# Optimization experiments

Hardware: AMD Instinct MI355X
Metric: run time of the kernel (lower is better)

The kernel has to match this reference:

```python
import jax, jax.numpy as jnp
import numpy as np
from jax.scipy.special import gammaln

# dims: S=state_dim, A=act_dim, H=horizon, HY=hyper_dim, B=batch, T=seq len
S, A, H, HY, B, T = 256, 16, 30, 64, 64, 64
EPS = 1e-6


def setup_inputs() -> dict:
    key = jax.random.key(0)
    ks = jax.random.split(key, 9)
    logp_o = jax.nn.log_softmax(jax.random.normal(ks[0], (T, B, S)), axis=-1)
    logp_u = jax.nn.log_softmax(jax.random.normal(ks[1], (T, B, A)), axis=-1)
    value = jax.random.normal(ks[2], (H, B, A, S))
    z = jax.random.normal(ks[3], (B, HY))
    b = jax.nn.softmax(jax.random.normal(ks[4], (B, S)), axis=-1)
    # learned parameters (xavier-ish scales, matching torch init magnitudes)
    w = jax.random.normal(ks[5], (1, A, S, S)) * (2.0 / (S + S)) ** 0.5
    w_offset_w = jax.random.normal(ks[6], (A * S * S, HY)) * 0.01  # Linear weight * 0.1
    tau = jax.random.uniform(ks[7], (1, 1), minval=-1.0, maxval=1.0)
    tau_offset_w = jax.random.normal(ks[8], (1, HY)) * 0.01
    return {"logp_o": logp_o, "logp_u": logp_u, "value": value, "z": z, "b": b,
            "w": w, "w_offset_w": w_offset_w, "tau": tau, "tau_offset_w": tau_offset_w}


def rectify(x):
    # positive rate; clipped exp for numerical safety
    return jnp.exp(jnp.clip(x, -8.0, 8.0))


def poisson_pdf(rate, K):
    # truncated, renormalized Poisson pmf over horizons 1..K; rate: [B,1] -> [B,K]
    ks = jnp.arange(1, K + 1, dtype=rate.dtype)
    logp = ks * jnp.log(rate) - rate - gammaln(ks + 1.0)
    return jax.nn.softmax(logp, axis=-1)


def reference(logp_o, logp_u, value, z, b, w, w_offset_w, tau, tau_offset_w):
    # compute_transition: hyper-offset + base full-rank weights, softmax over next-state
    w_off = (z @ w_offset_w.T).reshape(B, A, S, S)
    transition = jax.nn.softmax(w_off + w, axis=-1)  # [B,A,S,S]

    # compute_horizon_dist
    rate = rectify(tau + z @ tau_offset_w.T)  # [B,1]
    h_dist = poisson_pdf(rate, H)             # [B,H]

    # update_action for all timesteps at once
    alpha_a = jax.nn.softmax(logp_u, axis=-1)  # [T,B,A]

    def plan(b_t):
        # [B,S] x [H,B,A,S] -> [H,B,A]
        logits = jnp.einsum('bi,hbki->hbk', b_t, value)
        a = jax.nn.softmax(logits, axis=-1)
        return jnp.einsum('hbk,bh->bk', a, h_dist)  # [B,A]

    def step(b_t, inp):
        lo_t, a_t = inp
        # update_belief
        s_next = jnp.einsum('bkij,bi,bk->bj', transition, b_t, a_t)  # [B,S]
        b_next = jax.nn.softmax(jnp.log(s_next + EPS) + lo_t, axis=-1)
        return b_next, (b_next, plan(b_next))

    _, (alpha_b, alpha_pi) = jax.lax.scan(step, b, (logp_o, alpha_a))
    return alpha_b, alpha_pi  # [T,B,S], [T,B,A]
```

## Files before the change

### kernel.cpp

```cpp
#include <hip/hip_runtime.h>
#include <hip/hip_fp16.h>

#define DS 256
#define DA 16
#define DH 30
#define DHY 64
#define DB 64
#define DT 64

union HV  { int4 i4; __half2 h2[4]; };
union HV2 { int2 i2; __half2 h2[2]; };
typedef _Float16 f16x8 __attribute__((ext_vector_type(8)));
typedef float f32x4 __attribute__((ext_vector_type(4)));


__global__ __launch_bounds__(64) void k_hdist(const float* __restrict__ z,
                                              const float* __restrict__ tau,
                                              const float* __restrict__ tauw,
                                              float* __restrict__ h_dist) {
  const int bb = threadIdx.x;
  if (bb >= DB) return;
  float x = tau[0];
  for (int hy = 0; hy < DHY; ++hy) x = fmaf(z[bb * DHY + hy], tauw[hy], x);
  x = fminf(fmaxf(x, -8.f), 8.f);
  const float rate = __expf(x);
  const float lr = x;
  float lp[DH];
  float lg = 0.f;
  float mx = -1e30f;
  #pragma unroll
  for (int h = 0; h < DH; ++h) {
    const float ks = (float)(h + 1);
    lg += __logf(ks);
    lp[h] = ks * lr - rate - lg;
    mx = fmaxf(mx, lp[h]);
  }
  float sum = 0.f;
  #pragma unroll
  for (int h = 0; h < DH; ++h) { lp[h] = __expf(lp[h] - mx); sum += lp[h]; }
  const float inv = 1.f / sum;
  #pragma unroll
  for (int h = 0; h < DH; ++h) h_dist[bb * DH + h] = lp[h] * inv;
}

__global__ __launch_bounds__(256) void k_zf16(const float* __restrict__ z,
                                              _Float16* __restrict__ zf) {
  const int i = blockIdx.x * 256 + threadIdx.x;
  if (i < DB * DHY) zf[i] = (_Float16)z[i];
}

__global__ __launch_bounds__(256) void k_alpha(const float* __restrict__ logp_u,
                                               float* __restrict__ alpha_a) {
  const int row = blockIdx.x * 16 + (threadIdx.x >> 4);
  const int k = threadIdx.x & 15;
  const float v = logp_u[(size_t)row * DA + k];
  float m = v;
  #pragma unroll
  for (int o = 8; o >= 1; o >>= 1) m = fmaxf(m, __shfl_xor(m, o, 16));
  const float e = __expf(v - m);
  float s = e;
  #pragma unroll
  for (int o = 8; o >= 1; o >>= 1) s += __shfl_xor(s, o, 16);
  alpha_a[(size_t)row * DA + k] = e / s;
}

__global__ __launch_bounds__(256) void k_zero(float* __restrict__ out_pi) {
  out_pi[blockIdx.x * 256 + threadIdx.x] = 0.f;
}

__global__ __launch_bounds__(256) void k_vconv(const float* __restrict__ v,
                                               __half* __restrict__ v16, int n4) {
  const int stride = gridDim.x * 256;
  for (int i = blockIdx.x * 256 + threadIdx.x; i < n4; i += stride) {
    const float4 f = reinterpret_cast<const float4*>(v)[i];
    reinterpret_cast<__half2*>(v16)[2 * i]     = __floats2half2_rn(f.x, f.y);
    reinterpret_cast<__half2*>(v16)[2 * i + 1] = __floats2half2_rn(f.z, f.w);
  }
}

__global__ __launch_bounds__(256) void k_trans(const float* __restrict__ w,
                                               const float* __restrict__ wofs,
                                               const _Float16* __restrict__ zf,
                                               __half* __restrict__ trans) {
  const int ki = blockIdx.x;
  const int t = threadIdx.x;
  const int l = t & 63;
  const int wv = t >> 6;
  __shared__ __align__(16) char smem[32 * 1024];

  {
    const float* wrow = wofs + (size_t)ki * (DS * DHY);
    const int q = t & 3;
    #pragma unroll
    for (int pass = 0; pass < 4; ++pass) {
      const int j = pass * 64 + (t >> 2);
      const float4* src = reinterpret_cast<const float4*>(wrow + (size_t)j * DHY + q * 16);
      const float4 f0 = src[0], f1 = src[1], f2 = src[2], f3 = src[3];
      __half2 h[8];
      h[0] = __floats2half2_rn(f0.x, f0.y); h[1] = __floats2half2_rn(f0.z, f0.w);
      h[2] = __floats2half2_rn(f1.x, f1.y); h[3] = __floats2half2_rn(f1.z, f1.w);
      h[4] = __floats2half2_rn(f2.x, f2.y); h[5] = __floats2half2_rn(f2.z, f2.w);
      h[6] = __floats2half2_rn(f3.x, f3.y); h[7] = __floats2half2_rn(f3.z, f3.w);
      const int4* hv = reinterpret_cast<const int4*>(h);
      int b0 = j * 128 + (q * 2) * 16;     b0 ^= ((j & 7) << 4);
      int b1 = j * 128 + (q * 2 + 1) * 16; b1 ^= ((j & 7) << 4);
      *reinterpret_cast<int4*>(smem + b0) = hv[0];
      *reinterpret_cast<int4*>(smem + b1) = hv[1];
    }
  }
  __syncthreads();

  const int bcol = wv * 16 + (l & 15);
  const f16x8 Bf0 = *reinterpret_cast<const f16x8*>(zf + bcol * DHY + 0  + (l >> 4) * 8);
  const f16x8 Bf1 = *reinterpret_cast<const f16x8*>(zf + bcol * DHY + 32 + (l >> 4) * 8);

  f32x4 acc[16];
  #pragma unroll
  for (int m = 0; m < 16; ++m) {
    const int row0 = m * 16 + (l >> 4) * 4;
    const float4 w4 = *reinterpret_cast<const float4*>(w + (size_t)ki * DS + row0);
    acc[m][0] = w4.x; acc[m][1] = w4.y; acc[m][2] = w4.z; acc[m][3] = w4.w;
  }
  #pragma unroll
  for (int m = 0; m < 16; ++m) {
    const int row = m * 16 + (l & 15);
    int ba = row * 128 + (l >> 4) * 16;        ba ^= ((row & 7) << 4);
    int bb = row * 128 + (4 + (l >> 4)) * 16;  bb ^= ((row & 7) << 4);
    const f16x8 a0 = *reinterpret_cast<const f16x8*>(smem + ba);
    const f16x8 a1 = *reinterpret_cast<const f16x8*>(smem + bb);
    acc[m] = __builtin_amdgcn_mfma_f32_16x16x32_f16(a0, Bf0, acc[m], 0, 0, 0);
    acc[m] = __builtin_amdgcn_mfma_f32_16x16x32_f16(a1, Bf1, acc[m], 0, 0, 0);
  }

  float ssum = 0.f;
  #pragma unroll
  for (int m = 0; m < 16; ++m) {
    acc[m][0] = __expf(acc[m][0]); acc[m][1] = __expf(acc[m][1]);
    acc[m][2] = __expf(acc[m][2]); acc[m][3] = __expf(acc[m][3]);
    ssum += (acc[m][0] + acc[m][1]) + (acc[m][2] + acc[m][3]);
  }
  ssum += __shfl_xor(ssum, 16, 64);
  ssum += __shfl_xor(ssum, 32, 64);
  const float inv = 1.f / ssum;

  __half* tb = trans + (size_t)bcol * (DA * DS * DS) + (size_t)ki * DS;
  #pragma unroll
  for (int m = 0; m < 16; ++m) {
    const int j0 = m * 16 + (l >> 4) * 4;
    union { int2 i2; __half2 h[2]; } o;
    o.h[0] = __floats2half2_rn(acc[m][0] * inv, acc[m][1] * inv);
    o.h[1] = __floats2half2_rn(acc[m][2] * inv, acc[m][3] * inv);
    *reinterpret_cast<int2*>(tb + j0) = o.i2;
  }
}

__global__ __launch_bounds__(256) void k_mbuild(const __half* __restrict__ trans,
                                                const float* __restrict__ alpha_a,
                                                __half* __restrict__ Mch,
                                                int t0, int TC) {
  const int b = blockIdx.x >> 4;
  const int ich = (blockIdx.x & 15) << 4;
  const int tid = threadIdx.x;
  const int lane = tid & 63;
  const int wid = tid >> 6;
  __shared__ __half2 a_lds[16 * DA];
  for (int r = tid; r < TC * DA; r += 256)
    a_lds[r] = __float2half2_rn(alpha_a[((size_t)(t0 + (r >> 4)) * DB + b) * DA + (r & 15)]);
  __syncthreads();
  for (int io = 0; io < 4; ++io) {
    const int i = ich + io * 4 + wid;
    const __half* tp = trans + ((size_t)b * DA * DS + i) * DS + lane * 4;
    __half2 T2[32];
    #pragma unroll
    for (int k = 0; k < 16; ++k) {
      HV2 u;
      u.i2 = *reinterpret_cast<const int2*>(tp + (size_t)k * (DS * DS));
      T2[2 * k]     = u.h2[0];
      T2[2 * k + 1] = u.h2[1];
    }
    const __half2 z2 = __float2half2_rn(0.f);
    for (int tt = 0; tt < TC; ++tt) {
      __half2 m0 = z2, m1 = z2;
      #pragma unroll
      for (int k = 0; k < 16; ++k) {
        const __half2 ak = a_lds[tt * DA + k];
        m0 = __hfma2(ak, T2[2 * k], m0);
        m1 = __hfma2(ak, T2[2 * k + 1], m1);
      }
      HV2 o;
      o.h2[0] = m0;
      o.h2[1] = m1;
      *reinterpret_cast<int2*>(Mch + (((size_t)tt * DB + b) * DS + i) * DS + lane * 4) = o.i2;
    }
  }
}

#define LBAR() asm volatile("s_waitcnt lgkmcnt(0)\n\ts_barrier" ::: "memory")

#define SC_ISSUE(S, T)                                                          \
  if ((T) < TC) {                                                               \
    const __half* mb_ = Mch + (((size_t)(T) * DB + b) << 16) + jg * 8;          \
    S##0 = *reinterpret_cast<const int4*>(mb_ + (size_t)(iq + 0 * 32) * DS);    \
    S##1 = *reinterpret_cast<const int4*>(mb_ + (size_t)(iq + 1 * 32) * DS);    \
    S##2 = *reinterpret_cast<const int4*>(mb_ + (size_t)(iq + 2 * 32) * DS);    \
    S##3 = *reinterpret_cast<const int4*>(mb_ + (size_t)(iq + 3 * 32) * DS);    \
    S##4 = *reinterpret_cast<const int4*>(mb_ + (size_t)(iq + 4 * 32) * DS);    \
    S##5 = *reinterpret_cast<const int4*>(mb_ + (size_t)(iq + 5 * 32) * DS);    \
    S##6 = *reinterpret_cast<const int4*>(mb_ + (size_t)(iq + 6 * 32) * DS);    \
    S##7 = *reinterpret_cast<const int4*>(mb_ + (size_t)(iq + 7 * 32) * DS);    \
    if (tid < 64) lo_##S = *reinterpret_cast<const float4*>(                    \
        logp_o + ((size_t)(t0 + (T)) * DB + b) * DS + tid * 4);                 \
  }

#define SC_ACC1(Q, IT) {                                                 \
    const float wgt = bl[(IT) * 32 + iq];                                \
    HV u; u.i4 = (Q);                                                    \
    const float2 f0 = __half22float2(u.h2[0]);                           \
    const float2 f1 = __half22float2(u.h2[1]);                           \
    const float2 f2 = __half22float2(u.h2[2]);                           \
    const float2 f3 = __half22float2(u.h2[3]);                           \
    acc0 = fmaf(wgt, f0.x, acc0); acc1 = fmaf(wgt, f0.y, acc1);          \
    acc2 = fmaf(wgt, f1.x, acc2); acc3 = fmaf(wgt, f1.y, acc3);          \
    acc4 = fmaf(wgt, f2.x, acc4); acc5 = fmaf(wgt, f2.y, acc5);          \
    acc6 = fmaf(wgt, f3.x, acc6); acc7 = fmaf(wgt, f3.y, acc7); }

#define SC_STEP(S, T) {                                                  \
    float acc0=0.f,acc1=0.f,acc2=0.f,acc3=0.f,acc4=0.f,acc5=0.f,acc6=0.f,acc7=0.f; \
    SC_ACC1(S##0, 0) SC_ACC1(S##1, 1) SC_ACC1(S##2, 2) SC_ACC1(S##3, 3)  \
    SC_ACC1(S##4, 4) SC_ACC1(S##5, 5) SC_ACC1(S##6, 6) SC_ACC1(S##7, 7)  \
    acc0 += __shfl_xor(acc0, 32, 64); acc1 += __shfl_xor(acc1, 32, 64);  \
    acc2 += __shfl_xor(acc2, 32, 64); acc3 += __shfl_xor(acc3, 32, 64);  \
    acc4 += __shfl_xor(acc4, 32, 64); acc5 += __shfl_xor(acc5, 32, 64);  \
    acc6 += __shfl_xor(acc6, 32, 64); acc7 += __shfl_xor(acc7, 32, 64);  \
    if (lane < 32) {                                                     \
      red[w][lane][0] = acc0; red[w][lane][1] = acc1;                    \
      red[w][lane][2] = acc2; red[w][lane][3] = acc3;                    \
      red[w][lane][4] = acc4; red[w][lane][5] = acc5;                    \
      red[w][lane][6] = acc6; red[w][lane][7] = acc7;                    \
    }                                                                    \
    const float4 loC = lo_##S;   \
    LBAR();                                  \
    SC_ISSUE(S, (T) + 2)                \
    if (tid < 64) {                                                      \
      const int jj = tid >> 1, q0 = (tid & 1) * 4;                       \
      float4 sv = {0.f, 0.f, 0.f, 0.f};                                  \
      _Pragma("unroll")                                                  \
      for (int w2 = 0; w2 < 16; ++w2) {                                  \
        const float4 r4 = *reinterpret_cast<const float4*>(&red[w2][jj][q0]); \
        sv.x += r4.x; sv.y += r4.y; sv.z += r4.z; sv.w += r4.w;          \
      }                                                                  \
      const float e0 = __expf(__logf(sv.x + 1e-6f) + loC.x);             \
      const float e1 = __expf(__logf(sv.y + 1e-6f) + loC.y);             \
      const float e2 = __expf(__logf(sv.z + 1e-6f) + loC.z);             \
      const float e3 = __expf(__logf(sv.w + 1e-6f) + loC.w);             \
      float ps = (e0 + e1) + (e2 + e3);                                  \
      ps += __shfl_xor(ps, 1, 64);  ps += __shfl_xor(ps, 2, 64);         \
      ps += __shfl_xor(ps, 4, 64);  ps += __shfl_xor(ps, 8, 64);         \
      ps += __shfl_xor(ps, 16, 64); ps += __shfl_xor(ps, 32, 64);        \
      const float inv = 1.f / ps;                                        \
      float4 p4;                                                         \
      p4.x = e0 * inv; p4.y = e1 * inv; p4.z = e2 * inv; p4.w = e3 * inv;\
      *reinterpret_cast<float4*>(&bl[tid * 4]) = p4;                     \
      *reinterpret_cast<float4*>(                                        \
          &out_b[((size_t)(t0 + (T)) * DB + b) * DS + tid * 4]) = p4;    \
    }                                                                    \
    LBAR();   }

__global__ __launch_bounds__(1024, 4) void k_scanchunk(
    const __half* __restrict__ Mch,
    const float* __restrict__ logp_o,
    const float* __restrict__ b0,
    float* __restrict__ bl_buf,
    float* __restrict__ out_b,
    int t0, int TC) {
  const int b = blockIdx.x;
  const int tid = threadIdx.x;
  const int lane = tid & 63;
  const int w = tid >> 6;
  const int jg = tid & 31;
  const int iq = tid >> 5;
  __shared__ __align__(16) float bl[DS];
  __shared__ __align__(16) float red[16][32][12];
  if (tid < DS) bl[tid] = (t0 == 0) ? b0[b * DS + tid] : bl_buf[b * DS + tid];
  __syncthreads();

  int4 A0, A1, A2, A3, A4, A5, A6, A7;
  int4 B0, B1, B2, B3, B4, B5, B6, B7;
  float4 lo_A = {0.f, 0.f, 0.f, 0.f}, lo_B = {0.f, 0.f, 0.f, 0.f};

  SC_ISSUE(A, 0)
  SC_ISSUE(B, 1)
  for (int tt = 0; tt < TC; tt += 2) {
    SC_STEP(A, tt)
    SC_STEP(B, tt + 1)
  }
  if (tid < DS) bl_buf[b * DS + tid] = bl[tid];
}

__global__ __launch_bounds__(256) void k_planall(const float* __restrict__ out_b,
                                                 const __half* __restrict__ value16,
                                                 const float* __restrict__ h_dist,
                                                 float* __restrict__ out_pi) {
  const int b = blockIdx.x >> 6;
  const int t = blockIdx.x & 63;
  const int tid = threadIdx.x;
  const int lane = tid & 63;
  const int wid = tid >> 6;
  __shared__ __align__(16) float bl[DS];
  __shared__ float api[DA];
  bl[tid] = out_b[((size_t)t * DB + b) * DS + tid];
  if (tid < DA) api[tid] = 0.f;
  __syncthreads();
  const int k = lane >> 2;
  const int q = lane & 3;
  for (int p = 0; p < 8; ++p) {
    const int h = p * 4 + wid;
    if (h < DH) {
      const __half* vr = value16 + (((size_t)h * DB + b) * DA + k) * DS + q * 64;
      const float* blq = bl + q * 64;
      float dot = 0.f;
      #pragma unroll
      for (int ii = 0; ii < 64; ii += 8) {
        HV u;
        u.i4 = *reinterpret_cast<const int4*>(vr + ii);
        const float4 c0 = *reinterpret_cast<const float4*>(blq + ii);
        const float4 c1 = *reinterpret_cast<const float4*>(blq + ii + 4);
        const float2 f0 = __half22float2(u.h2[0]);
        const float2 f1 = __half22float2(u.h2[1]);
        const float2 f2 = __half22float2(u.h2[2]);
        const float2 f3 = __half22float2(u.h2[3]);
        dot = fmaf(f0.x, c0.x, dot); dot = fmaf(f0.y, c0.y, dot);
        dot = fmaf(f1.x, c0.z, dot); dot = fmaf(f1.y, c0.w, dot);
        dot = fmaf(f2.x, c1.x, dot); dot = fmaf(f2.y, c1.y, dot);
        dot = fmaf(f3.x, c1.z, dot); dot = fmaf(f3.y, c1.w, dot);
      }
      dot += __shfl_xor(dot, 1, 64);
      dot += __shfl_xor(dot, 2, 64);
      float mk = dot;
      #pragma unroll
      for (int o = 4; o <= 32; o <<= 1) mk = fmaxf(mk, __shfl_xor(mk, o, 64));
      const float ek = __expf(dot - mk);
      float sk = ek;
      #pragma unroll
      for (int o = 4; o <= 32; o <<= 1) sk += __shfl_xor(sk, o, 64);
      if (q == 0) atomicAdd(&api[k], (ek / sk) * h_dist[b * DH + h]);
    }
  }
  __syncthreads();
  if (tid < DA) out_pi[((size_t)t * DB + b) * DA + tid] = api[tid];
}

#define K_LD(I) (*reinterpret_cast<const int4*>(tb + (size_t)((I) * 64 + rb) * DS))
#define K_FMA(QV, I) {                                              \
    HV u; u.i4 = (QV);                                              \
    const float wgt = wv[(I) * 64 + rb];                            \
    const float2 f0 = __half22float2(u.h2[0]);                      \
    const float2 f1 = __half22float2(u.h2[1]);                      \
    const float2 f2 = __half22float2(u.h2[2]);                      \
    const float2 f3 = __half22float2(u.h2[3]);                      \
    acc[0] = fmaf(wgt, f0.x, acc[0]); acc[1] = fmaf(wgt, f0.y, acc[1]); \
    acc[2] = fmaf(wgt, f1.x, acc[2]); acc[3] = fmaf(wgt, f1.y, acc[3]); \
    acc[4] = fmaf(wgt, f2.x, acc[4]); acc[5] = fmaf(wgt, f2.y, acc[5]); \
    acc[6] = fmaf(wgt, f3.x, acc[6]); acc[7] = fmaf(wgt, f3.y, acc[7]); }

__global__ __launch_bounds__(256, 2) void k_step(
    const __half* __restrict__ trans, const float* __restrict__ logp_o,
    const float* __restrict__ logp_u, const __half* __restrict__ value16,
    const float* __restrict__ h_dist, const float* __restrict__ b0,
    float* __restrict__ s_buf, float* __restrict__ out_b,
    float* __restrict__ out_pi, int t) {
  const int bb = blockIdx.x & 63;
  const int jt = blockIdx.x >> 6;
  const int tid = threadIdx.x;
  const int lane = tid & 63;
  const int wid = tid >> 6;
  __shared__ __align__(16) float wv[DA * DS];
  __shared__ __align__(16) float bl[DS];
  __shared__ float aa[DA];
  __shared__ float redm[4], reds[4];
  __shared__ float red4[4][4][8];
  __shared__ float api[DA];
  if (t > 0) {
    const int tp = t - 1;
    const float sv = s_buf[(size_t)(tp & 1) * DB * DS + bb * DS + tid];
    const float l = __logf(sv + 1e-6f) + logp_o[((size_t)tp * DB + bb) * DS + tid];
    float m = l;
    #pragma unroll
    for (int o = 32; o >= 1; o >>= 1) m = fmaxf(m, __shfl_xor(m, o, 64));
    if (lane == 0) redm[wid] = m;
    __syncthreads();
    m = fmaxf(fmaxf(redm[0], redm[1]), fmaxf(redm[2], redm[3]));
    const float e = __expf(l - m);
    float v = e;
    #pragma unroll
    for (int o = 32; o >= 1; o >>= 1) v += __shfl_xor(v, o, 64);
    if (lane == 0) reds[wid] = v;
    if (tid < DA) api[tid] = 0.f;
    __syncthreads();
    const float p = e / (reds[0] + reds[1] + reds[2] + reds[3]);
    bl[tid] = p;
    if (jt == 0) out_b[((size_t)tp * DB + bb) * DS + tid] = p;
    __syncthreads();
    const int h = jt * 4 + wid;
    const int k = lane >> 2;
    const int q = lane & 3;
    if (h < DH) {
      const __half* vr = value16 + (((size_t)h * DB + bb) * DA + k) * DS + q * 64;
      const float* blq = bl + q * 64;
      float dot = 0.f;
      #pragma unroll
      for (int ii = 0; ii < 64; ii += 8) {
        HV u;
        u.i4 = *reinterpret_cast<const int4*>(vr + ii);
        const float4 c0 = *reinterpret_cast<const float4*>(blq + ii);
        const float4 c1 = *reinterpret_cast<const float4*>(blq + ii + 4);
        const float2 f0 = __half22float2(u.h2[0]);
        const float2 f1 = __half22float2(u.h2[1]);
        const float2 f2 = __half22float2(u.h2[2]);
        const float2 f3 = __half22float2(u.h2[3]);
        dot = fmaf(f0.x, c0.x, dot); dot = fmaf(f0.y, c0.y, dot);
        dot = fmaf(f1.x, c0.z, dot); dot = fmaf(f1.y, c0.w, dot);
        dot = fmaf(f2.x, c1.x, dot); dot = fmaf(f2.y, c1.y, dot);
        dot = fmaf(f3.x, c1.z, dot); dot = fmaf(f3.y, c1.w, dot);
      }
      dot += __shfl_xor(dot, 1, 64);
      dot += __shfl_xor(dot, 2, 64);
      float mk = dot;
      #pragma unroll
      for (int o = 4; o <= 32; o <<= 1) mk = fmaxf(mk, __shfl_xor(mk, o, 64));
      const float ek = __expf(dot - mk);
      float sk = ek;
      #pragma unroll
      for (int o = 4; o <= 32; o <<= 1) sk += __shfl_xor(sk, o, 64);
      if (q == 0) atomicAdd(&api[k], (ek / sk) * h_dist[bb * DH + h]);
    }
    __syncthreads();
    if (tid < DA) atomicAdd(&out_pi[((size_t)tp * DB + bb) * DA + tid], api[tid]);
  } else {
    bl[tid] = b0[bb * DS + tid];
  }
  __syncthreads();
  if (t < DT) {
    if (tid < DA) {
      const float lg = logp_u[((size_t)t * DB + bb) * DA + tid];
      float m = lg;
      #pragma unroll
      for (int o = 8; o >= 1; o >>= 1) m = fmaxf(m, __shfl_xor(m, o, 16));
      const float e = __expf(lg - m);
      float s = e;
      #pragma unroll
      for (int o = 8; o >= 1; o >>= 1) s += __shfl_xor(s, o, 16);
      aa[tid] = e / s;
    }
    __syncthreads();
    #pragma unroll
    for (int r = tid; r < DA * DS; r += 256) wv[r] = aa[r >> 8] * bl[r & 255];
    __syncthreads();
    const int jg = tid & 3;
    const int rb = tid >> 2;
    const __half* tb = trans + (size_t)bb * (DA * DS * DS) + jt * 32 + jg * 8;
    float acc[8] = {0.f, 0.f, 0.f, 0.f, 0.f, 0.f, 0.f, 0.f};
    int4 Q0 = K_LD(0), Q1 = K_LD(1), Q2 = K_LD(2), Q3 = K_LD(3);
    int4 Q4 = K_LD(4), Q5 = K_LD(5), Q6 = K_LD(6), Q7 = K_LD(7);
    #pragma unroll
    for (int it = 0; it < 56; it += 8) {
      K_FMA(Q0, it + 0); Q0 = K_LD(it + 8);
      K_FMA(Q1, it + 1); Q1 = K_LD(it + 9);
      K_FMA(Q2, it + 2); Q2 = K_LD(it + 10);
      K_FMA(Q3, it + 3); Q3 = K_LD(it + 11);
      K_FMA(Q4, it + 4); Q4 = K_LD(it + 12);
      K_FMA(Q5, it + 5); Q5 = K_LD(it + 13);
      K_FMA(Q6, it + 6); Q6 = K_LD(it + 14);
      K_FMA(Q7, it + 7); Q7 = K_LD(it + 15);
    }
    K_FMA(Q0, 56); K_FMA(Q1, 57); K_FMA(Q2, 58); K_FMA(Q3, 59);
    K_FMA(Q4, 60); K_FMA(Q5, 61); K_FMA(Q6, 62); K_FMA(Q7, 63);
    #pragma unroll
    for (int q = 0; q < 8; ++q) {
      acc[q] += __shfl_xor(acc[q], 4, 64);
      acc[q] += __shfl_xor(acc[q], 8, 64);
      acc[q] += __shfl_xor(acc[q], 16, 64);
      acc[q] += __shfl_xor(acc[q], 32, 64);
    }
    if (lane < 4) {
      #pragma unroll
      for (int q = 0; q < 8; ++q) red4[wid][lane][q] = acc[q];
    }
    __syncthreads();
    if (tid < 32) {
      const int jg2 = tid >> 3, q2 = tid & 7;
      const float s = red4[0][jg2][q2] + red4[1][jg2][q2] +
                      red4[2][jg2][q2] + red4[3][jg2][q2];
      s_buf[(size_t)(t & 1) * DB * DS + bb * DS + jt * 32 + jg2 * 8 + q2] = s;
    }
  }
}


extern "C" void kernel_launch(void* const* d_in, const int* in_sizes, int n_in,
                              void* d_out, int out_size, void* d_ws, size_t ws_size,
                              hipStream_t stream) {
  const float* logp_o = (const float*)d_in[0];
  const float* logp_u = (const float*)d_in[1];
  const float* value  = (const float*)d_in[2];
  const float* z      = (const float*)d_in[3];
  const float* b0     = (const float*)d_in[4];
  const float* w      = (const float*)d_in[5];
  const float* wofs   = (const float*)d_in[6];
  const float* tau    = (const float*)d_in[7];
  const float* tauw   = (const float*)d_in[8];

  char* ws = (char*)d_ws;
  size_t off = 0;
  __half* trans    = (__half*)(ws + off);    off += (size_t)DB * DA * DS * DS * sizeof(__half);
  __half* value16  = (__half*)(ws + off);    off += (size_t)DH * DB * DA * DS * sizeof(__half);
  float* alpha_a   = (float*)(ws + off);     off += (size_t)DT * DB * DA * sizeof(float);
  float* s_buf     = (float*)(ws + off);     off += (size_t)2 * DB * DS * sizeof(float);
  float* bl_buf    = (float*)(ws + off);     off += (size_t)DB * DS * sizeof(float);
  _Float16* zf16   = (_Float16*)(ws + off);  off += (size_t)DB * DHY * sizeof(_Float16);
  float* h_dist    = (float*)(ws + off);     off += 8192;
  const size_t base = off;
  if (base > ws_size) return;
  __half* M = (__half*)(ws + base);
  const size_t m_per_t = (size_t)DB * DS * DS * sizeof(__half);
  int TC = 0;
  const int cands[4] = {16, 8, 4, 2};
  for (int c = 0; c < 4; ++c)
    if (base + (size_t)cands[c] * m_per_t <= ws_size) { TC = cands[c]; break; }

  float* out_b  = (float*)d_out;
  float* out_pi = out_b + (size_t)DT * DB * DS;

  k_hdist<<<1, 64, 0, stream>>>(z, tau, tauw, h_dist);
  k_zf16<<<16, 256, 0, stream>>>(z, zf16);
  k_vconv<<<1024, 256, 0, stream>>>(value, value16, DH * DB * DA * DS / 4);
  k_trans<<<DA * DS, 256, 0, stream>>>(w, wofs, zf16, trans);

  if (TC) {
    k_alpha<<<256, 256, 0, stream>>>(logp_u, alpha_a);
    for (int c = 0; c < DT / TC; ++c) {
      k_mbuild<<<DB * 16, 256, 0, stream>>>(trans, alpha_a, M, c * TC, TC);
      k_scanchunk<<<DB, 1024, 0, stream>>>(M, logp_o, b0, bl_buf, out_b, c * TC, TC);
    }
    k_planall<<<DT * DB, 256, 0, stream>>>(out_b, value16, h_dist, out_pi);
  } else {
    k_zero<<<256, 256, 0, stream>>>(out_pi);
    for (int t = 0; t <= DT; ++t) {
      k_step<<<512, 256, 0, stream>>>(trans, logp_o, logp_u, value16, h_dist, b0,
                                      s_buf, out_b, out_pi, t);
    }
  }
}
```

Measured before the change: 608.6 us.

## Fuse M-build, scan, and plan into one software-pipelined chunk kernel

Replaces the alternating k_mbuild/k_scanchunk launches and the final k_planall with a single k_chunk kernel launched per chunk. Within each launch, 64 blocks scan chunk c, 256 blocks build the M matrices for chunk c+1 into a double buffer, and 128 blocks compute the plan outputs for chunk c-1. This overlaps the bandwidth-heavy M construction and the planning with the latency-bound serial scan, and it cuts the launch count. In exchange it fixes the chunk size at 8 and needs two M buffers, with different work types sharing 1024-thread blocks.

```diff
diff --git a/kernel.cpp b/kernel.cpp
--- a/kernel.cpp
+++ b/kernel.cpp
@@ -7,6 +7,7 @@
 #define DHY 64
 #define DB 64
 #define DT 64
+#define TCF 8
 
 union HV  { int4 i4; __half2 h2[4]; };
 union HV2 { int2 i2; __half2 h2[2]; };
@@ -154,51 +155,10 @@
   }
 }
 
-__global__ __launch_bounds__(256) void k_mbuild(const __half* __restrict__ trans,
-                                                const float* __restrict__ alpha_a,
-                                                __half* __restrict__ Mch,
-                                                int t0, int TC) {
-  const int b = blockIdx.x >> 4;
-  const int ich = (blockIdx.x & 15) << 4;
-  const int tid = threadIdx.x;
-  const int lane = tid & 63;
-  const int wid = tid >> 6;
-  __shared__ __half2 a_lds[16 * DA];
-  for (int r = tid; r < TC * DA; r += 256)
-    a_lds[r] = __float2half2_rn(alpha_a[((size_t)(t0 + (r >> 4)) * DB + b) * DA + (r & 15)]);
-  __syncthreads();
-  for (int io = 0; io < 4; ++io) {
-    const int i = ich + io * 4 + wid;
-    const __half* tp = trans + ((size_t)b * DA * DS + i) * DS + lane * 4;
-    __half2 T2[32];
-    #pragma unroll
-    for (int k = 0; k < 16; ++k) {
-      HV2 u;
-      u.i2 = *reinterpret_cast<const int2*>(tp + (size_t)k * (DS * DS));
-      T2[2 * k]     = u.h2[0];
-      T2[2 * k + 1] = u.h2[1];
-    }
-    const __half2 z2 = __float2half2_rn(0.f);
-    for (int tt = 0; tt < TC; ++tt) {
-      __half2 m0 = z2, m1 = z2;
-      #pragma unroll
-      for (int k = 0; k < 16; ++k) {
-        const __half2 ak = a_lds[tt * DA + k];
-        m0 = __hfma2(ak, T2[2 * k], m0);
-        m1 = __hfma2(ak, T2[2 * k + 1], m1);
-      }
-      HV2 o;
-      o.h2[0] = m0;
-      o.h2[1] = m1;
-      *reinterpret_cast<int2*>(Mch + (((size_t)tt * DB + b) * DS + i) * DS + lane * 4) = o.i2;
-    }
-  }
-}
-
 #define LBAR() asm volatile("s_waitcnt lgkmcnt(0)\n\ts_barrier" ::: "memory")
 
 #define SC_ISSUE(S, T)                                                          \
-  if ((T) < TC) {                                                               \
+  if ((T) < TCF) {                                                              \
     const __half* mb_ = Mch + (((size_t)(T) * DB + b) << 16) + jg * 8;          \
     S##0 = *reinterpret_cast<const int4*>(mb_ + (size_t)(iq + 0 * 32) * DS);    \
     S##1 = *reinterpret_cast<const int4*>(mb_ + (size_t)(iq + 1 * 32) * DS);    \
@@ -266,88 +226,140 @@
     }                                                                    \
     LBAR();   }
 
-__global__ __launch_bounds__(1024, 4) void k_scanchunk(
-    const __half* __restrict__ Mch,
+__global__ __launch_bounds__(1024, 4) void k_chunk(
+    const __half* __restrict__ trans,
+    const float* __restrict__ alpha_a,
     const float* __restrict__ logp_o,
+    const __half* __restrict__ value16,
+    const float* __restrict__ h_dist,
     const float* __restrict__ b0,
+    __half* __restrict__ M,
     float* __restrict__ bl_buf,
     float* __restrict__ out_b,
-    int t0, int TC) {
-  const int b = blockIdx.x;
+    float* __restrict__ out_pi,
+    int c) {
+  const int wg = blockIdx.x;
   const int tid = threadIdx.x;
   const int lane = tid & 63;
   const int w = tid >> 6;
-  const int jg = tid & 31;
-  const int iq = tid >> 5;
+
   __shared__ __align__(16) float bl[DS];
   __shared__ __align__(16) float red[16][32][12];
-  if (tid < DS) bl[tid] = (t0 == 0) ? b0[b * DS + tid] : bl_buf[b * DS + tid];
-  __syncthreads();
-
-  int4 A0, A1, A2, A3, A4, A5, A6, A7;
-  int4 B0, B1, B2, B3, B4, B5, B6, B7;
-  float4 lo_A = {0.f, 0.f, 0.f, 0.f}, lo_B = {0.f, 0.f, 0.f, 0.f};
-
-  SC_ISSUE(A, 0)
-  SC_ISSUE(B, 1)
-  for (int tt = 0; tt < TC; tt += 2) {
-    SC_STEP(A, tt)
-    SC_STEP(B, tt + 1)
-  }
-  if (tid < DS) bl_buf[b * DS + tid] = bl[tid];
-}
-
-__global__ __launch_bounds__(256) void k_planall(const float* __restrict__ out_b,
-                                                 const __half* __restrict__ value16,
-                                                 const float* __restrict__ h_dist,
-                                                 float* __restrict__ out_pi) {
-  const int b = blockIdx.x >> 6;
-  const int t = blockIdx.x & 63;
-  const int tid = threadIdx.x;
-  const int lane = tid & 63;
-  const int wid = tid >> 6;
-  __shared__ __align__(16) float bl[DS];
-  __shared__ float api[DA];
-  bl[tid] = out_b[((size_t)t * DB + b) * DS + tid];
-  if (tid < DA) api[tid] = 0.f;
-  __syncthreads();
-  const int k = lane >> 2;
-  const int q = lane & 3;
-  for (int p = 0; p < 8; ++p) {
-    const int h = p * 4 + wid;
-    if (h < DH) {
-      const __half* vr = value16 + (((size_t)h * DB + b) * DA + k) * DS + q * 64;
-      const float* blq = bl + q * 64;
-      float dot = 0.f;
-      #pragma unroll
-      for (int ii = 0; ii < 64; ii += 8) {
-        HV u;
-        u.i4 = *reinterpret_cast<const int4*>(vr + ii);
-        const float4 c0 = *reinterpret_cast<const float4*>(blq + ii);
-        const float4 c1 = *reinterpret_cast<const float4*>(blq + ii + 4);
-        const float2 f0 = __half22float2(u.h2[0]);
-        const float2 f1 = __half22float2(u.h2[1]);
-        const float2 f2 = __half22float2(u.h2[2]);
-        const float2 f3 = __half22float2(u.h2[3]);
-        dot = fmaf(f0.x, c0.x, dot); dot = fmaf(f0.y, c0.y, dot);
-        dot = fmaf(f1.x, c0.z, dot); dot = fmaf(f1.y, c0.w, dot);
-        dot = fmaf(f2.x, c1.x, dot); dot = fmaf(f2.y, c1.y, dot);
-        dot = fmaf(f3.x, c1.z, dot); dot = fmaf(f3.y, c1.w, dot);
+  __shared__ __half2 a_lds[TCF * DA];
+  __shared__ __align__(16) float bl4[4][DS];
+  __shared__ float api4[4][DA];
+
+  const size_t m_half = (size_t)TCF * DB * DS * DS;
+
+  if (wg < 64) {
+    if (c < 0 || c >= DT / TCF) return;
+    const int b = wg;
+    const int t0 = c * TCF;
+    const __half* Mch = M + (size_t)(c & 1) * m_half;
+    const int jg = tid & 31;
+    const int iq = tid >> 5;
+    if (tid < DS) bl[tid] = (t0 == 0) ? b0[b * DS + tid] : bl_buf[b * DS + tid];
+    __syncthreads();
+    int4 A0, A1, A2, A3, A4, A5, A6, A7;
+    int4 B0, B1, B2, B3, B4, B5, B6, B7;
+    float4 lo_A = {0.f, 0.f, 0.f, 0.f}, lo_B = {0.f, 0.f, 0.f, 0.f};
+    SC_ISSUE(A, 0)
+    SC_ISSUE(B, 1)
+    #pragma unroll
+    for (int tt = 0; tt < TCF; tt += 2) {
+      SC_STEP(A, tt)
+      SC_STEP(B, tt + 1)
+    }
+    if (tid < DS) bl_buf[b * DS + tid] = bl[tid];
+  } else if (wg < 320) {
+    const int cn = c + 1;
+    if (cn < 0 || cn >= DT / TCF) return;
+    const int wgm = wg - 64;
+    const int b = wgm >> 2;
+    const int ich = (wgm & 3) << 6;
+    const int t0 = cn * TCF;
+    __half* Mw = M + (size_t)(cn & 1) * m_half;
+    if (tid < TCF * DA)
+      a_lds[tid] = __float2half2_rn(alpha_a[((size_t)(t0 + (tid >> 4)) * DB + b) * DA + (tid & 15)]);
+    __syncthreads();
+    #pragma unroll 1
+    for (int io = 0; io < 4; ++io) {
+      const int i = ich + io * 16 + w;
+      const __half* tp = trans + ((size_t)b * DA * DS + i) * DS + lane * 4;
+      __half2 T2[32];
+      #pragma unroll
+      for (int k = 0; k < 16; ++k) {
+        HV2 u;
+        u.i2 = *reinterpret_cast<const int2*>(tp + (size_t)k * (DS * DS));
+        T2[2 * k]     = u.h2[0];
+        T2[2 * k + 1] = u.h2[1];
       }
-      dot += __shfl_xor(dot, 1, 64);
-      dot += __shfl_xor(dot, 2, 64);
-      float mk = dot;
-      #pragma unroll
-      for (int o = 4; o <= 32; o <<= 1) mk = fmaxf(mk, __shfl_xor(mk, o, 64));
-      const float ek = __expf(dot - mk);
-      float sk = ek;
-      #pragma unroll
-      for (int o = 4; o <= 32; o <<= 1) sk += __shfl_xor(sk, o, 64);
-      if (q == 0) atomicAdd(&api[k], (ek / sk) * h_dist[b * DH + h]);
-    }
-  }
-  __syncthreads();
-  if (tid < DA) out_pi[((size_t)t * DB + b) * DA + tid] = api[tid];
+      const __half2 z2 = __float2half2_rn(0.f);
+      #pragma unroll
+      for (int tt = 0; tt < TCF; ++tt) {
+        __half2 m0 = z2, m1 = z2;
+        #pragma unroll
+        for (int k = 0; k < 16; ++k) {
+          const __half2 ak = a_lds[tt * DA + k];
+          m0 = __hfma2(ak, T2[2 * k], m0);
+          m1 = __hfma2(ak, T2[2 * k + 1], m1);
+        }
+        HV2 o;
+        o.h2[0] = m0;
+        o.h2[1] = m1;
+        *reinterpret_cast<int2*>(Mw + (((size_t)tt * DB + b) * DS + i) * DS + lane * 4) = o.i2;
+      }
+    }
+  } else {
+    const int cp = c - 1;
+    if (cp < 0 || cp >= DT / TCF) return;
+    const int sub = tid >> 8;
+    const int tid2 = tid & 255;
+    const int pair = (wg - 320) * 4 + sub;
+    const int b = pair >> 3;
+    const int t = cp * TCF + (pair & 7);
+    const int wid2 = (tid2 >> 6);
+    bl4[sub][tid2] = out_b[((size_t)t * DB + b) * DS + tid2];
+    if (tid2 < DA) api4[sub][tid2] = 0.f;
+    __syncthreads();
+    const int k = lane >> 2;
+    const int q = lane & 3;
+    for (int p = 0; p < 8; ++p) {
+      const int h = p * 4 + wid2;
+      if (h < DH) {
+        const __half* vr = value16 + (((size_t)h * DB + b) * DA + k) * DS + q * 64;
+        const float* blq = &bl4[sub][q * 64];
+        float dot = 0.f;
+        #pragma unroll
+        for (int ii = 0; ii < 64; ii += 8) {
+          HV u;
+          u.i4 = *reinterpret_cast<const int4*>(vr + ii);
+          const float4 c0 = *reinterpret_cast<const float4*>(blq + ii);
+          const float4 c1 = *reinterpret_cast<const float4*>(blq + ii + 4);
+          const float2 f0 = __half22float2(u.h2[0]);
+          const float2 f1 = __half22float2(u.h2[1]);
+          const float2 f2 = __half22float2(u.h2[2]);
+          const float2 f3 = __half22float2(u.h2[3]);
+          dot = fmaf(f0.x, c0.x, dot); dot = fmaf(f0.y, c0.y, dot);
+          dot = fmaf(f1.x, c0.z, dot); dot = fmaf(f1.y, c0.w, dot);
+          dot = fmaf(f2.x, c1.x, dot); dot = fmaf(f2.y, c1.y, dot);
+          dot = fmaf(f3.x, c1.z, dot); dot = fmaf(f3.y, c1.w, dot);
+        }
+        dot += __shfl_xor(dot, 1, 64);
+        dot += __shfl_xor(dot, 2, 64);
+        float mk = dot;
+        #pragma unroll
+        for (int o = 4; o <= 32; o <<= 1) mk = fmaxf(mk, __shfl_xor(mk, o, 64));
+        const float ek = __expf(dot - mk);
+        float sk = ek;
+        #pragma unroll
+        for (int o = 4; o <= 32; o <<= 1) sk += __shfl_xor(sk, o, 64);
+        if (q == 0) atomicAdd(&api4[sub][k], (ek / sk) * h_dist[b * DH + h]);
+      }
+    }
+    __syncthreads();
+    if (tid2 < DA) out_pi[((size_t)t * DB + b) * DA + tid2] = api4[sub][tid2];
+  }
 }
 
 #define K_LD(I) (*reinterpret_cast<const int4*>(tb + (size_t)((I) * 64 + rb) * DS))
@@ -522,11 +534,8 @@
   const size_t base = off;
   if (base > ws_size) return;
   __half* M = (__half*)(ws + base);
-  const size_t m_per_t = (size_t)DB * DS * DS * sizeof(__half);
-  int TC = 0;
-  const int cands[4] = {16, 8, 4, 2};
-  for (int c = 0; c < 4; ++c)
-    if (base + (size_t)cands[c] * m_per_t <= ws_size) { TC = cands[c]; break; }
+  const size_t m_half = (size_t)TCF * DB * DS * DS * sizeof(__half);
+  const bool fused_ok = (base + 2 * m_half) <= ws_size;
 
   float* out_b  = (float*)d_out;
   float* out_pi = out_b + (size_t)DT * DB * DS;
@@ -536,13 +545,12 @@
   k_vconv<<<1024, 256, 0, stream>>>(value, value16, DH * DB * DA * DS / 4);
   k_trans<<<DA * DS, 256, 0, stream>>>(w, wofs, zf16, trans);
 
-  if (TC) {
+  if (fused_ok) {
     k_alpha<<<256, 256, 0, stream>>>(logp_u, alpha_a);
-    for (int c = 0; c < DT / TC; ++c) {
-      k_mbuild<<<DB * 16, 256, 0, stream>>>(trans, alpha_a, M, c * TC, TC);
-      k_scanchunk<<<DB, 1024, 0, stream>>>(M, logp_o, b0, bl_buf, out_b, c * TC, TC);
-    }
-    k_planall<<<DT * DB, 256, 0, stream>>>(out_b, value16, h_dist, out_pi);
+    for (int c = -1; c <= DT / TCF; ++c) {
+      k_chunk<<<448, 1024, 0, stream>>>(trans, alpha_a, logp_o, value16, h_dist,
+                                        b0, M, bl_buf, out_b, out_pi, c);
+    }
   } else {
     k_zero<<<256, 256, 0, stream>>>(out_pi);
     for (int t = 0; t <= DT; ++t) {
```

Result: slower. 1.045 ms (+71.7%).
